# Kernel tuning notes

Hardware: AMD Instinct MI355X
Metric: run time of the kernel (lower is better)

## Reference

```python
import jax, jax.numpy as jnp
import numpy as np

NUM_CLASSES = 10
N = 4194304  # 2**22 samples


def setup_inputs() -> dict:
    key = jax.random.key(0)
    k1, k2 = jax.random.split(key)
    outputs = jax.random.uniform(k1, (N, NUM_CLASSES), dtype=jnp.float32)
    target = jax.random.randint(k2, (N,), 0, NUM_CLASSES, dtype=jnp.int64)
    return {"outputs": outputs, "target": target}


def reference(outputs, target):
    # y = one-hot(target) with 10 classes, float
    y = jax.nn.one_hot(target, NUM_CLASSES, dtype=outputs.dtype)  # [N, 10]
    # sum_j (outputs @ y.T)[i, j] == outputs[i] . sum_j y[j]
    # identical math to torch.sum(torch.mm(outputs, y.t()), dim=1) without the [N, N] intermediate
    col_counts = jnp.sum(y, axis=0)                 # [10] class counts
    nominator = outputs @ col_counts                # [N]
    denominator = jnp.linalg.norm(outputs) * jnp.linalg.norm(y)  # Frobenius norms
    return jnp.mean(-jnp.log(nominator / denominator))
```

## Files before the change

### kernel.cpp

```cpp
#include <hip/hip_runtime.h>
#include <math.h>

#define NUM_CLASSES 10



__global__ void __launch_bounds__(256) hist_kernel(const int* __restrict__ target,
                                                   unsigned int* __restrict__ counts,
                                                   int n) {
    unsigned int cnt[NUM_CLASSES];
#pragma unroll
    for (int c = 0; c < NUM_CLASSES; ++c) cnt[c] = 0u;

    const int tid = blockIdx.x * blockDim.x + threadIdx.x;
    const int stride = gridDim.x * blockDim.x;
    const int4* __restrict__ t4 = (const int4*)target;
    const int n4 = n >> 2;

    for (int i = tid; i < n4; i += stride) {
        int4 v = t4[i];
#pragma unroll
        for (int c = 0; c < NUM_CLASSES; ++c) {
            cnt[c] += (unsigned int)(v.x == c) + (unsigned int)(v.y == c) +
                      (unsigned int)(v.z == c) + (unsigned int)(v.w == c);
        }
    }

#pragma unroll
    for (int c = 0; c < NUM_CLASSES; ++c) {
        unsigned int v = cnt[c];
        for (int off = 32; off > 0; off >>= 1)
            v += (unsigned int)__shfl_down((int)v, off, 64);
        cnt[c] = v;
    }

    __shared__ unsigned int sh[NUM_CLASSES];
    if (threadIdx.x < NUM_CLASSES) sh[threadIdx.x] = 0u;
    __syncthreads();
    if ((threadIdx.x & 63) == 0) {
#pragma unroll
        for (int c = 0; c < NUM_CLASSES; ++c)
            atomicAdd(&sh[c], cnt[c]);
    }
    __syncthreads();
    if (threadIdx.x < NUM_CLASSES)
        atomicAdd(&counts[threadIdx.x], sh[threadIdx.x]);
}

__global__ void __launch_bounds__(256) main_kernel(const float* __restrict__ outputs,
                                                   const unsigned int* __restrict__ counts_u,
                                                   float* __restrict__ acc,
                                                   int n) {
    float w[NUM_CLASSES];
#pragma unroll
    for (int c = 0; c < NUM_CLASSES; ++c) w[c] = (float)counts_u[c];

    const int tid = blockIdx.x * blockDim.x + threadIdx.x;
    const int stride = gridDim.x * blockDim.x;
    const int npairs = n >> 1;
    const float4* __restrict__ o4 = (const float4*)outputs;

    float sum_log = 0.f, sumsq = 0.f;
    for (int p = tid; p < npairs; p += stride) {
        const float4* base = o4 + (size_t)p * 5;
        float4 a = base[0];
        float4 b = base[1];
        float4 c4 = base[2];
        float4 d = base[3];
        float4 e = base[4];
        float r0[NUM_CLASSES] = {a.x, a.y, a.z, a.w, b.x, b.y, b.z, b.w, c4.x, c4.y};
        float r1[NUM_CLASSES] = {c4.z, c4.w, d.x, d.y, d.z, d.w, e.x, e.y, e.z, e.w};
        float nom0 = 0.f, nom1 = 0.f;
#pragma unroll
        for (int c = 0; c < NUM_CLASSES; ++c) {
            nom0 += r0[c] * w[c];
            nom1 += r1[c] * w[c];
            sumsq += r0[c] * r0[c] + r1[c] * r1[c];
        }
        sum_log += __logf(nom0) + __logf(nom1);
    }

    for (int off = 32; off > 0; off >>= 1) {
        sum_log += __shfl_down(sum_log, off, 64);
        sumsq   += __shfl_down(sumsq, off, 64);
    }
    __shared__ float s1[4], s2[4];
    const int wave = threadIdx.x >> 6;
    if ((threadIdx.x & 63) == 0) { s1[wave] = sum_log; s2[wave] = sumsq; }
    __syncthreads();
    if (threadIdx.x == 0) {
        float t1 = 0.f, t2 = 0.f;
        for (int wv = 0; wv < 4; ++wv) { t1 += s1[wv]; t2 += s2[wv]; }
        atomicAdd(&acc[0], t1);
        atomicAdd(&acc[1], t2);
    }
}

__global__ void finalize_kernel(const float* __restrict__ acc, float* __restrict__ out, float fn) {
    if (threadIdx.x == 0 && blockIdx.x == 0) {
        out[0] = 0.5f * logf(acc[1]) + 0.5f * logf(fn) - acc[0] / fn;
    }
}

extern "C" void kernel_launch(void* const* d_in, const int* in_sizes, int n_in,
                              void* d_out, int out_size, void* d_ws, size_t ws_size,
                              hipStream_t stream) {
    const float* outputs = (const float*)d_in[0];
    const int* target = (const int*)d_in[1];
    const int n = in_sizes[1];

    unsigned int* counts = (unsigned int*)d_ws;
    float* acc = (float*)((char*)d_ws + NUM_CLASSES * sizeof(unsigned int));

    hipMemsetAsync(d_ws, 0, (NUM_CLASSES + 2) * sizeof(unsigned int), stream);
    hist_kernel<<<512, 256, 0, stream>>>(target, counts, n);
    main_kernel<<<2048, 256, 0, stream>>>(outputs, counts, acc, n);
    finalize_kernel<<<1, 64, 0, stream>>>(acc, (float*)d_out, (float)n);
}
```

Before: 267.2 us.

## Coalesce output loads via LDS staging and replace atomics with per-block partials

The main kernel now has each wave load a contiguous 128-row chunk with fully coalesced float4 reads and stage it through shared memory before computing per-row dot products. The old per-thread layout made strided 80-byte reads. Global atomics and the memset are replaced with per-block partial arrays: each main block re-reduces the 512 histogram partials, and the finalize kernel sums the 2048 main partials. This adds two block barriers per iteration, plus redundant histogram reduction in every block.

```diff
diff --git a/kernel.cpp b/kernel.cpp
--- a/kernel.cpp
+++ b/kernel.cpp
@@ -2,12 +2,12 @@
 #include <math.h>
 
 #define NUM_CLASSES 10
-
+#define A_BLOCKS 512
+#define B_BLOCKS 2048
 
 
 __global__ void __launch_bounds__(256) hist_kernel(const int* __restrict__ target,
-                                                   unsigned int* __restrict__ counts,
-                                                   int n) {
+                                                   unsigned int* __restrict__ pc, int n) {
     unsigned int cnt[NUM_CLASSES];
 #pragma unroll
     for (int c = 0; c < NUM_CLASSES; ++c) cnt[c] = 0u;
@@ -34,71 +34,136 @@
         cnt[c] = v;
     }
 
-    __shared__ unsigned int sh[NUM_CLASSES];
-    if (threadIdx.x < NUM_CLASSES) sh[threadIdx.x] = 0u;
-    __syncthreads();
+    __shared__ unsigned int sh[4][NUM_CLASSES];
+    const int wave = threadIdx.x >> 6;
     if ((threadIdx.x & 63) == 0) {
 #pragma unroll
-        for (int c = 0; c < NUM_CLASSES; ++c)
-            atomicAdd(&sh[c], cnt[c]);
+        for (int c = 0; c < NUM_CLASSES; ++c) sh[wave][c] = cnt[c];
     }
     __syncthreads();
-    if (threadIdx.x < NUM_CLASSES)
-        atomicAdd(&counts[threadIdx.x], sh[threadIdx.x]);
+    if (threadIdx.x < NUM_CLASSES) {
+        const int c = threadIdx.x;
+        pc[blockIdx.x * NUM_CLASSES + c] = sh[0][c] + sh[1][c] + sh[2][c] + sh[3][c];
+    }
 }
 
 __global__ void __launch_bounds__(256) main_kernel(const float* __restrict__ outputs,
-                                                   const unsigned int* __restrict__ counts_u,
-                                                   float* __restrict__ acc,
-                                                   int n) {
+                                                   const unsigned int* __restrict__ pc,
+                                                   float2* __restrict__ pacc, int n) {
+    const int wave = threadIdx.x >> 6;
+    const int lane = threadIdx.x & 63;
+
+    unsigned int pw[NUM_CLASSES];
+#pragma unroll
+    for (int c = 0; c < NUM_CLASSES; ++c) pw[c] = 0u;
+#pragma unroll
+    for (int r = 0; r < A_BLOCKS / 256; ++r) {
+        const unsigned int* row = pc + (threadIdx.x + r * 256) * NUM_CLASSES;
+#pragma unroll
+        for (int c = 0; c < NUM_CLASSES; ++c) pw[c] += row[c];
+    }
+#pragma unroll
+    for (int c = 0; c < NUM_CLASSES; ++c) {
+        unsigned int v = pw[c];
+        for (int off = 32; off > 0; off >>= 1)
+            v += (unsigned int)__shfl_down((int)v, off, 64);
+        pw[c] = v;
+    }
+    __shared__ unsigned int shw[4][NUM_CLASSES];
+    __shared__ float fw[NUM_CLASSES];
+    if (lane == 0) {
+#pragma unroll
+        for (int c = 0; c < NUM_CLASSES; ++c) shw[wave][c] = pw[c];
+    }
+    __syncthreads();
+    if (threadIdx.x < NUM_CLASSES) {
+        const int c = threadIdx.x;
+        fw[c] = (float)(shw[0][c] + shw[1][c] + shw[2][c] + shw[3][c]);
+    }
+    __syncthreads();
     float w[NUM_CLASSES];
 #pragma unroll
-    for (int c = 0; c < NUM_CLASSES; ++c) w[c] = (float)counts_u[c];
+    for (int c = 0; c < NUM_CLASSES; ++c) w[c] = fw[c];
 
-    const int tid = blockIdx.x * blockDim.x + threadIdx.x;
-    const int stride = gridDim.x * blockDim.x;
-    const int npairs = n >> 1;
+    __shared__ float4 stage4[4][320];
     const float4* __restrict__ o4 = (const float4*)outputs;
+    const int nchunks = n >> 7;
+    const int nwaves = gridDim.x * 4;
+    const int gwave = blockIdx.x * 4 + wave;
+    const int iters = (nchunks + nwaves - 1) / nwaves;
 
     float sum_log = 0.f, sumsq = 0.f;
-    for (int p = tid; p < npairs; p += stride) {
-        const float4* base = o4 + (size_t)p * 5;
-        float4 a = base[0];
-        float4 b = base[1];
-        float4 c4 = base[2];
-        float4 d = base[3];
-        float4 e = base[4];
-        float r0[NUM_CLASSES] = {a.x, a.y, a.z, a.w, b.x, b.y, b.z, b.w, c4.x, c4.y};
-        float r1[NUM_CLASSES] = {c4.z, c4.w, d.x, d.y, d.z, d.w, e.x, e.y, e.z, e.w};
-        float nom0 = 0.f, nom1 = 0.f;
+    for (int it = 0; it < iters; ++it) {
+        const int ch = gwave + it * nwaves;
+        const bool valid = ch < nchunks;
+        float4 v0, v1, v2, v3, v4;
+        if (valid) {
+            const size_t b4 = (size_t)ch * 320;
+            v0 = o4[b4 + 0 * 64 + lane];
+            v1 = o4[b4 + 1 * 64 + lane];
+            v2 = o4[b4 + 2 * 64 + lane];
+            v3 = o4[b4 + 3 * 64 + lane];
+            v4 = o4[b4 + 4 * 64 + lane];
+        }
+        __syncthreads();
+        if (valid) {
+            stage4[wave][0 * 64 + lane] = v0;
+            stage4[wave][1 * 64 + lane] = v1;
+            stage4[wave][2 * 64 + lane] = v2;
+            stage4[wave][3 * 64 + lane] = v3;
+            stage4[wave][4 * 64 + lane] = v4;
+        }
+        __syncthreads();
+        if (valid) {
+            const float4* sp = (const float4*)((const float*)&stage4[wave][0] + lane * 20);
+            float4 a = sp[0], b = sp[1], c4 = sp[2], d = sp[3], e = sp[4];
+            float r0[NUM_CLASSES] = {a.x, a.y, a.z, a.w, b.x, b.y, b.z, b.w, c4.x, c4.y};
+            float r1[NUM_CLASSES] = {c4.z, c4.w, d.x, d.y, d.z, d.w, e.x, e.y, e.z, e.w};
+            float nom0 = 0.f, nom1 = 0.f;
 #pragma unroll
-        for (int c = 0; c < NUM_CLASSES; ++c) {
-            nom0 += r0[c] * w[c];
-            nom1 += r1[c] * w[c];
-            sumsq += r0[c] * r0[c] + r1[c] * r1[c];
+            for (int c = 0; c < NUM_CLASSES; ++c) {
+                nom0 += r0[c] * w[c];
+                nom1 += r1[c] * w[c];
+                sumsq += r0[c] * r0[c] + r1[c] * r1[c];
+            }
+            sum_log += __logf(nom0) + __logf(nom1);
         }
-        sum_log += __logf(nom0) + __logf(nom1);
     }
 
     for (int off = 32; off > 0; off >>= 1) {
         sum_log += __shfl_down(sum_log, off, 64);
-        sumsq   += __shfl_down(sumsq, off, 64);
+        sumsq += __shfl_down(sumsq, off, 64);
+    }
+    __shared__ float s1[4], s2[4];
+    if (lane == 0) { s1[wave] = sum_log; s2[wave] = sumsq; }
+    __syncthreads();
+    if (threadIdx.x == 0) {
+        float t1 = s1[0] + s1[1] + s1[2] + s1[3];
+        float t2 = s2[0] + s2[1] + s2[2] + s2[3];
+        pacc[blockIdx.x] = make_float2(t1, t2);
+    }
+}
+
+__global__ void __launch_bounds__(256) finalize_kernel(const float2* __restrict__ pacc,
+                                                       float* __restrict__ out, float fn) {
+    float sum_log = 0.f, sumsq = 0.f;
+    for (int i = threadIdx.x; i < B_BLOCKS; i += 256) {
+        float2 v = pacc[i];
+        sum_log += v.x;
+        sumsq += v.y;
+    }
+    for (int off = 32; off > 0; off >>= 1) {
+        sum_log += __shfl_down(sum_log, off, 64);
+        sumsq += __shfl_down(sumsq, off, 64);
     }
     __shared__ float s1[4], s2[4];
     const int wave = threadIdx.x >> 6;
     if ((threadIdx.x & 63) == 0) { s1[wave] = sum_log; s2[wave] = sumsq; }
     __syncthreads();
     if (threadIdx.x == 0) {
-        float t1 = 0.f, t2 = 0.f;
-        for (int wv = 0; wv < 4; ++wv) { t1 += s1[wv]; t2 += s2[wv]; }
-        atomicAdd(&acc[0], t1);
-        atomicAdd(&acc[1], t2);
-    }
-}
-
-__global__ void finalize_kernel(const float* __restrict__ acc, float* __restrict__ out, float fn) {
-    if (threadIdx.x == 0 && blockIdx.x == 0) {
-        out[0] = 0.5f * logf(acc[1]) + 0.5f * logf(fn) - acc[0] / fn;
+        float t1 = s1[0] + s1[1] + s1[2] + s1[3];
+        float t2 = s2[0] + s2[1] + s2[2] + s2[3];
+        out[0] = 0.5f * logf(t2) + 0.5f * logf(fn) - t1 / fn;
     }
 }
 
@@ -109,11 +174,10 @@
     const int* target = (const int*)d_in[1];
     const int n = in_sizes[1];
 
-    unsigned int* counts = (unsigned int*)d_ws;
-    float* acc = (float*)((char*)d_ws + NUM_CLASSES * sizeof(unsigned int));
+    unsigned int* pc = (unsigned int*)d_ws;
+    float2* pacc = (float2*)((char*)d_ws + A_BLOCKS * NUM_CLASSES * sizeof(unsigned int));
 
-    hipMemsetAsync(d_ws, 0, (NUM_CLASSES + 2) * sizeof(unsigned int), stream);
-    hist_kernel<<<512, 256, 0, stream>>>(target, counts, n);
-    main_kernel<<<2048, 256, 0, stream>>>(outputs, counts, acc, n);
-    finalize_kernel<<<1, 64, 0, stream>>>(acc, (float*)d_out, (float)n);
+    hist_kernel<<<A_BLOCKS, 256, 0, stream>>>(target, pc, n);
+    main_kernel<<<B_BLOCKS, 256, 0, stream>>>(outputs, pc, pacc, n);
+    finalize_kernel<<<1, 256, 0, stream>>>(pacc, (float*)d_out, (float)n);
 }
```

Result: faster. 250.6 us (median of 2 runs) (-6.2%).
